# Optimization experiments

Hardware: AMD Instinct MI355X
Metric: run time of the kernel (lower is better)

The kernel has to match this reference:

```python
import jax, jax.numpy as jnp
import numpy as np

N, T, V, F, K, FO = 8, 64, 200, 64, 3, 64


def setup_inputs() -> dict:
    key = jax.random.key(0)
    k1, k2, k3, k4 = jax.random.split(key, 4)
    x = jax.random.normal(k1, (N, T, V, F), dtype=jnp.float32)
    Att = jax.random.uniform(k2, (N, V, V), dtype=jnp.float32)
    S = jax.random.uniform(k3, (N, T, V, V), dtype=jnp.float32)
    Theta = jax.random.normal(k4, (K, F, FO), dtype=jnp.float32) * 0.1
    return {"x": x, "Att": Att, "S": S, "Theta": Theta}


def reference(x, Att, S, Theta):
    # x: (N,T,V,F); Att: (N,V,V); S: (N,T,V,V); Theta: (K,F,FO)
    n, t, v, f = x.shape
    k_order = Theta.shape[0]
    # symmetrize S by elementwise min with its transpose (last two dims)
    S = jnp.minimum(S, jnp.swapaxes(S, -1, -2))
    eye = jnp.eye(v, dtype=x.dtype)
    # D = diag_embed(sum(A, dim=1)) per timestep -> column sums over axis 2
    d = jnp.sum(S, axis=2)                      # (N,T,V)
    L = d[..., :, None] * eye - S               # (N,T,V,V), D - A
    L_t = L - eye                               # tilde-L
    # Chebyshev recursion (elementwise, matching original code exactly)
    polys = [jnp.broadcast_to(eye, (1, 1, v, v)), L_t][:k_order]
    for _ in range(2, k_order):
        polys.append(2.0 * L_t * polys[-1] - polys[-2])
    Att_b = Att[:, None]                        # (N,1,V,V), broadcast over T
    out = jnp.zeros((n, t, v, Theta.shape[-1]), dtype=x.dtype)
    for kk in range(k_order):
        T_k_att = polys[kk] * Att_b             # (N,T,V,V) (broadcast for k=0)
        # rhs = T_k_att^T @ x : sum over vertex u
        rhs = jnp.einsum('...uv,...uf->...vf', T_k_att, x)  # (N,T,V,F)
        out = out + rhs @ Theta[kk]             # (N,T,V,FO)
    return jax.nn.relu(out)
```

## Files before the change

kernel.cpp:

```cpp
#include <hip/hip_runtime.h>

namespace {

typedef __attribute__((ext_vector_type(8)))  short          short8;
typedef __attribute__((ext_vector_type(8)))  unsigned short u16x8;
typedef __attribute__((ext_vector_type(4)))  unsigned short u16x4;
typedef __attribute__((ext_vector_type(4)))  float          f32x4;

constexpr int V   = 200;
constexpr int VP  = 208;
constexpr int UP  = 224;
constexpr int F   = 64;
constexpr int FO  = 64;
constexpr int NT  = 512;

constexpr int A_ROW = 448;

constexpr size_t WS_AC  = 0;
constexpr size_t WS_D   = 95420416;
constexpr size_t WS_SD  = 95846400;
constexpr size_t WS_AD  = 96272384;
constexpr size_t WS_THT = 96279552;

__device__ __forceinline__ unsigned short f2bf(float x) {
    union { float f; unsigned u; } c; c.f = x;
    unsigned r = c.u + 0x7FFF + ((c.u >> 16) & 1);
    return (unsigned short)(r >> 16);
}
__device__ __forceinline__ float bf2f(unsigned short h) {
    union { unsigned u; float f; } c; c.u = ((unsigned)h) << 16;
    return c.f;
}

__global__ __launch_bounds__(256)
void prep_A(const float* __restrict__ S,
            const float* __restrict__ Att,
            unsigned short* __restrict__ Ac,
            float* __restrict__ d_ws,
            float* __restrict__ sdiag)
{
    __shared__ float As[32][33];
    __shared__ float Bs[32][33];
    __shared__ float Ts[32][33];
    __shared__ float Us[32][33];

    const int b   = blockIdx.x;
    const int n   = b >> 6;
    const int tid = threadIdx.x;
    int rem = blockIdx.y, ti = 0;
    while (rem >= 7 - ti) { rem -= 7 - ti; ++ti; }
    const int tj = ti + rem;
    const bool diag = (ti == tj);

    const float* __restrict__ Sp = S   + (size_t)b * (V * V);
    const float* __restrict__ Ap = Att + (size_t)n * (V * V);

    const int r  = tid >> 3;
    const int cg = tid & 7;
    const int c0 = 4 * cg;

    {
        const int gr = 32 * ti + r, gc = 32 * tj + c0;
        float4 a = make_float4(0.f, 0.f, 0.f, 0.f);
        float4 t = make_float4(0.f, 0.f, 0.f, 0.f);
        if (gr < V && gc < V) {
            a = *(const float4*)&Sp[gr * V + gc];
            t = *(const float4*)&Ap[gr * V + gc];
        }
        As[r][c0 + 0] = a.x; As[r][c0 + 1] = a.y; As[r][c0 + 2] = a.z; As[r][c0 + 3] = a.w;
        Ts[r][c0 + 0] = t.x; Ts[r][c0 + 1] = t.y; Ts[r][c0 + 2] = t.z; Ts[r][c0 + 3] = t.w;
        if (!diag) {
            const int hr = 32 * tj + r, hc = 32 * ti + c0;
            float4 bb = make_float4(0.f, 0.f, 0.f, 0.f);
            float4 uu = make_float4(0.f, 0.f, 0.f, 0.f);
            if (hr < V && hc < V) {
                bb = *(const float4*)&Sp[hr * V + hc];
                uu = *(const float4*)&Ap[hr * V + hc];
            }
            Bs[r][c0 + 0] = bb.x; Bs[r][c0 + 1] = bb.y; Bs[r][c0 + 2] = bb.z; Bs[r][c0 + 3] = bb.w;
            Us[r][c0 + 0] = uu.x; Us[r][c0 + 1] = uu.y; Us[r][c0 + 2] = uu.z; Us[r][c0 + 3] = uu.w;
        }
    }
    __syncthreads();

    {
        const int vr = 32 * ti + r;
        float rs = 0.f;
        u16x4 w1, w2;
        #pragma unroll
        for (int e = 0; e < 4; ++e) {
            const int c = c0 + e;
            const float tw = diag ? As[c][r] : Bs[c][r];
            const float m  = fminf(As[r][c], tw);
            rs += m;
            const float att = diag ? Ts[c][r] : Us[c][r];
            float a1 = -m * att;
            float a2 = 2.0f * m * m * att;
            if (diag && r == c) { a1 = 0.f; a2 = 0.f; }
            w1[e] = f2bf(a1); w2[e] = f2bf(a2);
        }
        float s = rs;
        s += __shfl_xor(s, 1); s += __shfl_xor(s, 2); s += __shfl_xor(s, 4);
        if (cg == 0 && vr < V)
            atomicAdd(&d_ws[b * VP + vr], s);
        if (diag && cg == 0 && vr < V)
            sdiag[b * VP + vr] = As[r][r];
        if (vr < VP) {
            const size_t base = ((size_t)(b * VP + vr) * 7 + tj) * 64;
            *(u16x4*)&Ac[base + c0]      = w1;
            *(u16x4*)&Ac[base + 32 + c0] = w2;
        }
    }

    if (!diag) {
        const int vr2 = 32 * tj + r;
        float ts = 0.f;
        u16x4 w1, w2;
        #pragma unroll
        for (int e = 0; e < 4; ++e) {
            const int c = c0 + e;
            const float m = fminf(Bs[r][c], As[c][r]);
            ts += m;
            const float att = Ts[c][r];
            w1[e] = f2bf(-m * att);
            w2[e] = f2bf(2.0f * m * m * att);
        }
        float s = ts;
        s += __shfl_xor(s, 1); s += __shfl_xor(s, 2); s += __shfl_xor(s, 4);
        if (cg == 0 && vr2 < V)
            atomicAdd(&d_ws[b * VP + vr2], s);
        if (vr2 < VP) {
            const size_t base = ((size_t)(b * VP + vr2) * 7 + ti) * 64;
            *(u16x4*)&Ac[base + c0]      = w1;
            *(u16x4*)&Ac[base + 32 + c0] = w2;
        }
    }
}

__global__ __launch_bounds__(256)
void prep_adiag(const float* __restrict__ Att, float* __restrict__ adiag)
{
    const int n = blockIdx.x, tid = threadIdx.x;
    if (tid < UP)
        adiag[n * UP + tid] = (tid < V) ? Att[(size_t)n * (V * V) + tid * V + tid] : 0.f;
}

__global__ __launch_bounds__(256)
void prep_theta(const float* __restrict__ Theta,
                unsigned short* __restrict__ thT)
{
    __shared__ float T[64][65];
    const int k = blockIdx.x, tid = threadIdx.x;
    for (int idx = tid; idx < 4096; idx += 256)
        T[idx >> 6][idx & 63] = Theta[k * 4096 + idx];
    __syncthreads();
    for (int idx = tid; idx < 4096; idx += 256) {
        const int fo = idx >> 6, f = idx & 63;
        thT[k * 4096 + fo * 64 + f] = f2bf(T[f][fo]);
    }
}

constexpr int XS_S = 68;
constexpr int XT_S = 232;
constexpr int YS_S = 72;

__global__ __launch_bounds__(256, 2)
void cheb_main(const float* __restrict__ x,
               const unsigned short* __restrict__ thT,
               const unsigned short* __restrict__ Ac,
               const float* __restrict__ d_ws,
               const float* __restrict__ sdiag,
               const float* __restrict__ adiag,
               float* __restrict__ out)
{
    __shared__ __align__(16) char smem[61824];
    unsigned short* xsT = (unsigned short*)smem;
    unsigned short* xs  = (unsigned short*)(smem + 29696);
    unsigned short* ThS = (unsigned short*)smem;
    unsigned short* ys  = (unsigned short*)(smem + 29696);
    float*        cbuf  = (float*)(smem + 60160);
    float*       adbuf  = (float*)(smem + 60992);

    const int tid = threadIdx.x;
    const int b   = blockIdx.x;
    const int n   = b >> 6;
    const float* __restrict__ xp = x + (size_t)b * (V * F);
    const unsigned short* __restrict__ ap = Ac + (size_t)b * (VP * A_ROW);
    float* __restrict__ op = out + (size_t)b * (V * FO);

    for (int idx = tid; idx < UP * 16; idx += 256) {
        const int u = idx >> 4, fg = idx & 15;
        u16x4 w; w[0] = 0; w[1] = 0; w[2] = 0; w[3] = 0;
        if (u < V) {
            const float4 v = *(const float4*)&xp[u * F + 4 * fg];
            w[0] = f2bf(v.x); w[1] = f2bf(v.y); w[2] = f2bf(v.z); w[3] = f2bf(v.w);
        }
        *(u16x4*)&xs[u * XS_S + 4 * fg] = w;
    }
    if (tid < VP) {
        cbuf[tid]  = d_ws[b * VP + tid] - 1.0f - sdiag[b * VP + tid];
        adbuf[tid] = adiag[n * UP + tid];
    }
    __syncthreads();

    for (int it = 0; it < 7; ++it) {
        const int wid = tid + 256 * it;
        const int f = wid & 63, uc = wid >> 6;
        u16x8 w;
        #pragma unroll
        for (int j = 0; j < 8; ++j) w[j] = xs[(8 * uc + j) * XS_S + f];
        *(u16x8*)&xsT[f * XT_S + 8 * uc] = w;
    }
    __syncthreads();

    const int wave = tid >> 6, lane = tid & 63;
    const int q = lane >> 4, ln = lane & 15;
    const int myBase = (wave == 0) ? 0 : (4 + 3 * (wave - 1));
    const int myCnt  = (wave == 0) ? 4 : 3;

    f32x4 acc1[4][4], acc2[4][4];
    #pragma unroll
    for (int i = 0; i < 4; ++i)
        #pragma unroll
        for (int j = 0; j < 4; ++j) {
            acc1[i][j] = (f32x4)0.f; acc2[i][j] = (f32x4)0.f;
        }

    size_t rbase[4];
    #pragma unroll
    for (int vi = 0; vi < 4; ++vi)
        rbase[vi] = (size_t)((myBase + vi) * 16 + ln) * A_ROW;

    short8 a1c[4] = {}, a2c[4] = {}, a1n[4] = {}, a2n[4] = {};
    #pragma unroll
    for (int vi = 0; vi < 4; ++vi) if (vi < myCnt) {
        a1c[vi] = *(const short8*)&ap[rbase[vi] + 8 * q];
        a2c[vi] = *(const short8*)&ap[rbase[vi] + 32 + 8 * q];
    }
    #pragma unroll 1
    for (int kt = 0; kt < 7; ++kt) {
        if (kt < 6) {
            #pragma unroll
            for (int vi = 0; vi < 4; ++vi) if (vi < myCnt) {
                a1n[vi] = *(const short8*)&ap[rbase[vi] + (kt + 1) * 64 + 8 * q];
                a2n[vi] = *(const short8*)&ap[rbase[vi] + (kt + 1) * 64 + 32 + 8 * q];
            }
        }
        short8 bfr[4];
        #pragma unroll
        for (int ft = 0; ft < 4; ++ft)
            bfr[ft] = *(const short8*)&xsT[(16 * ft + ln) * XT_S + 32 * kt + 8 * q];
        #pragma unroll
        for (int vi = 0; vi < 4; ++vi) if (vi < myCnt) {
            #pragma unroll
            for (int ft = 0; ft < 4; ++ft) {
                acc1[vi][ft] = __builtin_amdgcn_mfma_f32_16x16x32_bf16(a1c[vi], bfr[ft], acc1[vi][ft], 0, 0, 0);
                acc2[vi][ft] = __builtin_amdgcn_mfma_f32_16x16x32_bf16(a2c[vi], bfr[ft], acc2[vi][ft], 0, 0, 0);
            }
        }
        #pragma unroll
        for (int vi = 0; vi < 4; ++vi) { a1c[vi] = a1n[vi]; a2c[vi] = a2n[vi]; }
    }

    f32x4 ot[4][4];
    #pragma unroll
    for (int i = 0; i < 4; ++i)
        #pragma unroll
        for (int j = 0; j < 4; ++j) ot[i][j] = (f32x4)0.f;

    #pragma unroll
    for (int pass = 0; pass < 3; ++pass) {
        const int k = (pass == 0) ? 1 : (pass == 1) ? 2 : 0;
        __syncthreads();

        if (k == 0) {
            for (int idx = tid; idx < VP * 16; idx += 256) {
                const int v = idx >> 4, fg = idx & 15;
                u16x4 w; w[0] = 0; w[1] = 0; w[2] = 0; w[3] = 0;
                if (v < V) {
                    const float av = adbuf[v];
                    const float4 xv = *(const float4*)&xp[v * F + 4 * fg];
                    w[0] = f2bf(av * xv.x); w[1] = f2bf(av * xv.y);
                    w[2] = f2bf(av * xv.z); w[3] = f2bf(av * xv.w);
                }
                *(u16x4*)&ys[v * YS_S + 4 * fg] = w;
            }
        } else {
            #pragma unroll
            for (int vi = 0; vi < 4; ++vi) {
                if (vi < myCnt) {
                    const int vt = myBase + vi;
                    #pragma unroll
                    for (int ft = 0; ft < 4; ++ft) {
                        const f32x4 a = (k == 1) ? acc1[vi][ft] : acc2[vi][ft];
                        #pragma unroll
                        for (int reg = 0; reg < 4; ++reg) {
                            const int v = vt * 16 + 4 * q + reg;
                            float val = 0.f;
                            if (v < V) {
                                const float cc = cbuf[v];
                                const float dc = ((k == 1) ? cc : (2.0f * cc * cc - 1.0f)) * adbuf[v];
                                val = a[reg] + dc * xp[v * F + 16 * ft + ln];
                            }
                            ys[v * YS_S + 16 * ft + ln] = f2bf(val);
                        }
                    }
                }
            }
        }
        for (int idx = tid; idx < 64 * 8; idx += 256) {
            const int fo = idx >> 3, ch = idx & 7;
            *(u16x8*)&ThS[fo * YS_S + 8 * ch] =
                *(const u16x8*)&thT[k * 4096 + fo * 64 + 8 * ch];
        }
        __syncthreads();
        #pragma unroll
        for (int vi = 0; vi < 4; ++vi) {
            if (vi < myCnt) {
                const int vrow = (myBase + vi) * 16 + ln;
                #pragma unroll
                for (int ks = 0; ks < 2; ++ks) {
                    const short8 af = *(const short8*)&ys[vrow * YS_S + 32 * ks + 8 * q];
                    #pragma unroll
                    for (int fot = 0; fot < 4; ++fot) {
                        const short8 bf = *(const short8*)&ThS[(16 * fot + ln) * YS_S + 32 * ks + 8 * q];
                        ot[vi][fot] = __builtin_amdgcn_mfma_f32_16x16x32_bf16(af, bf, ot[vi][fot], 0, 0, 0);
                    }
                }
            }
        }
    }

    #pragma unroll
    for (int vi = 0; vi < 4; ++vi) {
        if (vi < myCnt) {
            const int vt = myBase + vi;
            #pragma unroll
            for (int fot = 0; fot < 4; ++fot) {
                #pragma unroll
                for (int reg = 0; reg < 4; ++reg) {
                    const int v = vt * 16 + 4 * q + reg;
                    if (v < V)
                        op[v * FO + 16 * fot + ln] = fmaxf(ot[vi][fot][reg], 0.f);
                }
            }
        }
    }
}

}

extern "C" void kernel_launch(void* const* d_in, const int* in_sizes, int n_in,
                              void* d_out, int out_size, void* d_ws, size_t ws_size,
                              hipStream_t stream) {
    const float* x     = (const float*)d_in[0];
    const float* Att   = (const float*)d_in[1];
    const float* S     = (const float*)d_in[2];
    const float* Theta = (const float*)d_in[3];
    float* out         = (float*)d_out;

    char* ws = (char*)d_ws;
    unsigned short* Ac  = (unsigned short*)(ws + WS_AC);
    float* d_sum        = (float*)(ws + WS_D);
    float* sdiag        = (float*)(ws + WS_SD);
    float* adiag        = (float*)(ws + WS_AD);
    unsigned short* thT = (unsigned short*)(ws + WS_THT);

    hipMemsetAsync(d_sum, 0, (size_t)NT * VP * sizeof(float), stream);

    hipLaunchKernelGGL(prep_A,     dim3(NT, 28), dim3(256), 0, stream, S, Att, Ac, d_sum, sdiag);
    hipLaunchKernelGGL(prep_adiag, dim3(8),      dim3(256), 0, stream, Att, adiag);
    hipLaunchKernelGGL(prep_theta, dim3(3),      dim3(256), 0, stream, Theta, thT);
    hipLaunchKernelGGL(cheb_main,  dim3(NT),     dim3(256), 0, stream,
                       x, thT, Ac, d_sum, sdiag, adiag, out);
}
```

Measured before the change: 247.5 us.

## Fuse Laplacian/attention prep into main Chebyshev kernel, split vertices across two blocks

The separate prep_A pass, which wrote a large bf16 A matrix to workspace along with atomically summed degrees, is removed. Each block of the fused kernel now reads S and Att tiles directly, symmetrises them, builds the bf16 A1/A2 tiles in LDS and accumulates degree sums per 32-column chunk before issuing MFMAs. Each timestep is split across two blocks by vertex half, with smaller LDS and accumulator sets, targeting occupancy 4. x transposition and Theta preparation are merged into one small prep kernel. This avoids the workspace round-trip and the memset, but each block re-reads its S columns, and Att is read with strided scalar loads.

```diff
diff --git a/kernel.cpp b/kernel.cpp
--- a/kernel.cpp
+++ b/kernel.cpp
@@ -7,264 +7,205 @@
 typedef __attribute__((ext_vector_type(4)))  unsigned short u16x4;
 typedef __attribute__((ext_vector_type(4)))  float          f32x4;
 
-constexpr int V   = 200;
-constexpr int VP  = 208;
-constexpr int UP  = 224;
-constexpr int F   = 64;
-constexpr int FO  = 64;
-constexpr int NT  = 512;
-
-constexpr int A_ROW = 448;
-
-constexpr size_t WS_AC  = 0;
-constexpr size_t WS_D   = 95420416;
-constexpr size_t WS_SD  = 95846400;
-constexpr size_t WS_AD  = 96272384;
-constexpr size_t WS_THT = 96279552;
+constexpr int V  = 200;
+constexpr int F  = 64;
+constexpr int NT = 512;
+
+constexpr size_t WS_XT  = 0;
+constexpr size_t WS_THT = 14680064;
 
 __device__ __forceinline__ unsigned short f2bf(float x) {
     union { float f; unsigned u; } c; c.f = x;
     unsigned r = c.u + 0x7FFF + ((c.u >> 16) & 1);
     return (unsigned short)(r >> 16);
 }
-__device__ __forceinline__ float bf2f(unsigned short h) {
-    union { unsigned u; float f; } c; c.u = ((unsigned)h) << 16;
-    return c.f;
-}
 
 __global__ __launch_bounds__(256)
-void prep_A(const float* __restrict__ S,
-            const float* __restrict__ Att,
-            unsigned short* __restrict__ Ac,
-            float* __restrict__ d_ws,
-            float* __restrict__ sdiag)
+void prep_misc(const float* __restrict__ x,
+               const float* __restrict__ Theta,
+               unsigned short* __restrict__ xT,
+               unsigned short* __restrict__ thT)
 {
-    __shared__ float As[32][33];
-    __shared__ float Bs[32][33];
-    __shared__ float Ts[32][33];
-    __shared__ float Us[32][33];
-
-    const int b   = blockIdx.x;
-    const int n   = b >> 6;
+    __shared__ __align__(16) char smem[30464];
+    const int bb = blockIdx.x, tid = threadIdx.x;
+    if (bb < NT) {
+        unsigned short* xs = (unsigned short*)smem;
+        const float* __restrict__ xp = x + (size_t)bb * (V * F);
+        for (int idx = tid; idx < 224 * 16; idx += 256) {
+            const int u = idx >> 4, fg = idx & 15;
+            u16x4 w; w[0] = 0; w[1] = 0; w[2] = 0; w[3] = 0;
+            if (u < V) {
+                const float4 v4 = *(const float4*)&xp[u * F + 4 * fg];
+                w[0] = f2bf(v4.x); w[1] = f2bf(v4.y); w[2] = f2bf(v4.z); w[3] = f2bf(v4.w);
+            }
+            *(u16x4*)&xs[u * 68 + 4 * fg] = w;
+        }
+        __syncthreads();
+        unsigned short* xo = xT + (size_t)bb * (64 * 224);
+        for (int it = 0; it < 8; ++it) {
+            const int wid = tid + 256 * it;
+            const int f = wid >> 5, sl = wid & 31;
+            if (sl < 28) {
+                u16x8 w;
+                #pragma unroll
+                for (int j = 0; j < 8; ++j) w[j] = xs[(8 * sl + j) * 68 + f];
+                *(u16x8*)&xo[f * 224 + 8 * sl] = w;
+            }
+        }
+    } else {
+        float* T = (float*)smem;
+        for (int k = 0; k < 3; ++k) {
+            __syncthreads();
+            for (int idx = tid; idx < 4096; idx += 256)
+                T[(idx >> 6) * 65 + (idx & 63)] = Theta[k * 4096 + idx];
+            __syncthreads();
+            for (int idx = tid; idx < 4096; idx += 256) {
+                const int fo = idx >> 6, f = idx & 63;
+                thT[k * 4096 + fo * 64 + f] = f2bf(T[f * 65 + fo]);
+            }
+        }
+    }
+}
+
+__global__ __launch_bounds__(256, 4)
+void cheb_fused(const float* __restrict__ x,
+                const float* __restrict__ S,
+                const float* __restrict__ Att,
+                const unsigned short* __restrict__ thT,
+                const unsigned short* __restrict__ xT,
+                float* __restrict__ out)
+{
+    __shared__ __align__(16) char smem[30208];
+    float*          sru = (float*)smem;
+    unsigned short* A1  = (unsigned short*)(smem + 14464);
+    unsigned short* A2  = (unsigned short*)(smem + 21632);
+    unsigned short* ys  = (unsigned short*)smem;
+    unsigned short* ThS = (unsigned short*)(smem + 16128);
+    float* dbuf = (float*)(smem + 28800);
+    float* sdb  = (float*)(smem + 29248);
+    float* adb  = (float*)(smem + 29696);
+
     const int tid = threadIdx.x;
-    int rem = blockIdx.y, ti = 0;
-    while (rem >= 7 - ti) { rem -= 7 - ti; ++ti; }
-    const int tj = ti + rem;
-    const bool diag = (ti == tj);
-
-    const float* __restrict__ Sp = S   + (size_t)b * (V * V);
-    const float* __restrict__ Ap = Att + (size_t)n * (V * V);
-
-    const int r  = tid >> 3;
-    const int cg = tid & 7;
-    const int c0 = 4 * cg;
-
-    {
-        const int gr = 32 * ti + r, gc = 32 * tj + c0;
-        float4 a = make_float4(0.f, 0.f, 0.f, 0.f);
-        float4 t = make_float4(0.f, 0.f, 0.f, 0.f);
-        if (gr < V && gc < V) {
-            a = *(const float4*)&Sp[gr * V + gc];
-            t = *(const float4*)&Ap[gr * V + gc];
-        }
-        As[r][c0 + 0] = a.x; As[r][c0 + 1] = a.y; As[r][c0 + 2] = a.z; As[r][c0 + 3] = a.w;
-        Ts[r][c0 + 0] = t.x; Ts[r][c0 + 1] = t.y; Ts[r][c0 + 2] = t.z; Ts[r][c0 + 3] = t.w;
-        if (!diag) {
-            const int hr = 32 * tj + r, hc = 32 * ti + c0;
-            float4 bb = make_float4(0.f, 0.f, 0.f, 0.f);
-            float4 uu = make_float4(0.f, 0.f, 0.f, 0.f);
-            if (hr < V && hc < V) {
-                bb = *(const float4*)&Sp[hr * V + hc];
-                uu = *(const float4*)&Ap[hr * V + hc];
-            }
-            Bs[r][c0 + 0] = bb.x; Bs[r][c0 + 1] = bb.y; Bs[r][c0 + 2] = bb.z; Bs[r][c0 + 3] = bb.w;
-            Us[r][c0 + 0] = uu.x; Us[r][c0 + 1] = uu.y; Us[r][c0 + 2] = uu.z; Us[r][c0 + 3] = uu.w;
-        }
-    }
+    const int b = blockIdx.x >> 1, h = blockIdx.x & 1;
+    const int n = b >> 6;
+    const int v0 = h * 112;
+    const int NVL = h ? 96 : 112;
+    const int NV4 = NVL >> 2;
+
+    const float* __restrict__ Sp  = S   + (size_t)b * (V * V);
+    const float* __restrict__ Ap  = Att + (size_t)n * (V * V);
+    const float* __restrict__ xp  = x   + (size_t)b * (V * F);
+    const unsigned short* __restrict__ xTp = xT + (size_t)b * (64 * 224);
+    float* __restrict__ op = out + (size_t)b * (V * F);
+
+    if (tid < 112) { dbuf[tid] = 0.f; sdb[tid] = 0.f; adb[tid] = 0.f; }
+
+    const int wave = tid >> 6, lane = tid & 63, q = lane >> 4, ln = lane & 15;
+    int myBase, myCnt;
+    if (h == 0) { myCnt = (wave < 3) ? 2 : 1; myBase = 2 * wave; }
+    else        { myCnt = (wave < 2) ? 2 : 1; myBase = (wave < 2) ? 2 * wave : 2 + wave; }
+
+    f32x4 acc1[2][4], acc2[2][4];
+    #pragma unroll
+    for (int i = 0; i < 2; ++i)
+        #pragma unroll
+        for (int j = 0; j < 4; ++j) { acc1[i][j] = (f32x4)0.f; acc2[i][j] = (f32x4)0.f; }
+
+    float4 spf[4];
+    auto load_sru = [&](int kt) {
+        #pragma unroll
+        for (int c = 0; c < 4; ++c) {
+            const int idx = tid + 256 * c;
+            const int ul = idx >> 5, sl = idx & 31;
+            const int u = 32 * kt + ul, vv = v0 + 4 * sl;
+            float4 z = make_float4(0.f, 0.f, 0.f, 0.f);
+            if (sl < NV4 && u < V && vv < V)
+                z = *(const float4*)&Sp[u * V + vv];
+            spf[c] = z;
+        }
+    };
+    load_sru(0);
     __syncthreads();
 
-    {
-        const int vr = 32 * ti + r;
-        float rs = 0.f;
-        u16x4 w1, w2;
-        #pragma unroll
-        for (int e = 0; e < 4; ++e) {
-            const int c = c0 + e;
-            const float tw = diag ? As[c][r] : Bs[c][r];
-            const float m  = fminf(As[r][c], tw);
-            rs += m;
-            const float att = diag ? Ts[c][r] : Us[c][r];
-            float a1 = -m * att;
-            float a2 = 2.0f * m * m * att;
-            if (diag && r == c) { a1 = 0.f; a2 = 0.f; }
-            w1[e] = f2bf(a1); w2[e] = f2bf(a2);
-        }
-        float s = rs;
-        s += __shfl_xor(s, 1); s += __shfl_xor(s, 2); s += __shfl_xor(s, 4);
-        if (cg == 0 && vr < V)
-            atomicAdd(&d_ws[b * VP + vr], s);
-        if (diag && cg == 0 && vr < V)
-            sdiag[b * VP + vr] = As[r][r];
-        if (vr < VP) {
-            const size_t base = ((size_t)(b * VP + vr) * 7 + tj) * 64;
-            *(u16x4*)&Ac[base + c0]      = w1;
-            *(u16x4*)&Ac[base + 32 + c0] = w2;
-        }
-    }
-
-    if (!diag) {
-        const int vr2 = 32 * tj + r;
-        float ts = 0.f;
-        u16x4 w1, w2;
-        #pragma unroll
-        for (int e = 0; e < 4; ++e) {
-            const int c = c0 + e;
-            const float m = fminf(Bs[r][c], As[c][r]);
-            ts += m;
-            const float att = Ts[c][r];
-            w1[e] = f2bf(-m * att);
-            w2[e] = f2bf(2.0f * m * m * att);
-        }
-        float s = ts;
-        s += __shfl_xor(s, 1); s += __shfl_xor(s, 2); s += __shfl_xor(s, 4);
-        if (cg == 0 && vr2 < V)
-            atomicAdd(&d_ws[b * VP + vr2], s);
-        if (vr2 < VP) {
-            const size_t base = ((size_t)(b * VP + vr2) * 7 + ti) * 64;
-            *(u16x4*)&Ac[base + c0]      = w1;
-            *(u16x4*)&Ac[base + 32 + c0] = w2;
-        }
-    }
-}
-
-__global__ __launch_bounds__(256)
-void prep_adiag(const float* __restrict__ Att, float* __restrict__ adiag)
-{
-    const int n = blockIdx.x, tid = threadIdx.x;
-    if (tid < UP)
-        adiag[n * UP + tid] = (tid < V) ? Att[(size_t)n * (V * V) + tid * V + tid] : 0.f;
-}
-
-__global__ __launch_bounds__(256)
-void prep_theta(const float* __restrict__ Theta,
-                unsigned short* __restrict__ thT)
-{
-    __shared__ float T[64][65];
-    const int k = blockIdx.x, tid = threadIdx.x;
-    for (int idx = tid; idx < 4096; idx += 256)
-        T[idx >> 6][idx & 63] = Theta[k * 4096 + idx];
-    __syncthreads();
-    for (int idx = tid; idx < 4096; idx += 256) {
-        const int fo = idx >> 6, f = idx & 63;
-        thT[k * 4096 + fo * 64 + f] = f2bf(T[f][fo]);
-    }
-}
-
-constexpr int XS_S = 68;
-constexpr int XT_S = 232;
-constexpr int YS_S = 72;
-
-__global__ __launch_bounds__(256, 2)
-void cheb_main(const float* __restrict__ x,
-               const unsigned short* __restrict__ thT,
-               const unsigned short* __restrict__ Ac,
-               const float* __restrict__ d_ws,
-               const float* __restrict__ sdiag,
-               const float* __restrict__ adiag,
-               float* __restrict__ out)
-{
-    __shared__ __align__(16) char smem[61824];
-    unsigned short* xsT = (unsigned short*)smem;
-    unsigned short* xs  = (unsigned short*)(smem + 29696);
-    unsigned short* ThS = (unsigned short*)smem;
-    unsigned short* ys  = (unsigned short*)(smem + 29696);
-    float*        cbuf  = (float*)(smem + 60160);
-    float*       adbuf  = (float*)(smem + 60992);
-
-    const int tid = threadIdx.x;
-    const int b   = blockIdx.x;
-    const int n   = b >> 6;
-    const float* __restrict__ xp = x + (size_t)b * (V * F);
-    const unsigned short* __restrict__ ap = Ac + (size_t)b * (VP * A_ROW);
-    float* __restrict__ op = out + (size_t)b * (V * FO);
-
-    for (int idx = tid; idx < UP * 16; idx += 256) {
-        const int u = idx >> 4, fg = idx & 15;
-        u16x4 w; w[0] = 0; w[1] = 0; w[2] = 0; w[3] = 0;
-        if (u < V) {
-            const float4 v = *(const float4*)&xp[u * F + 4 * fg];
-            w[0] = f2bf(v.x); w[1] = f2bf(v.y); w[2] = f2bf(v.z); w[3] = f2bf(v.w);
-        }
-        *(u16x4*)&xs[u * XS_S + 4 * fg] = w;
-    }
-    if (tid < VP) {
-        cbuf[tid]  = d_ws[b * VP + tid] - 1.0f - sdiag[b * VP + tid];
-        adbuf[tid] = adiag[n * UP + tid];
-    }
-    __syncthreads();
-
-    for (int it = 0; it < 7; ++it) {
-        const int wid = tid + 256 * it;
-        const int f = wid & 63, uc = wid >> 6;
-        u16x8 w;
-        #pragma unroll
-        for (int j = 0; j < 8; ++j) w[j] = xs[(8 * uc + j) * XS_S + f];
-        *(u16x8*)&xsT[f * XT_S + 8 * uc] = w;
-    }
-    __syncthreads();
-
-    const int wave = tid >> 6, lane = tid & 63;
-    const int q = lane >> 4, ln = lane & 15;
-    const int myBase = (wave == 0) ? 0 : (4 + 3 * (wave - 1));
-    const int myCnt  = (wave == 0) ? 4 : 3;
-
-    f32x4 acc1[4][4], acc2[4][4];
-    #pragma unroll
-    for (int i = 0; i < 4; ++i)
-        #pragma unroll
-        for (int j = 0; j < 4; ++j) {
-            acc1[i][j] = (f32x4)0.f; acc2[i][j] = (f32x4)0.f;
-        }
-
-    size_t rbase[4];
-    #pragma unroll
-    for (int vi = 0; vi < 4; ++vi)
-        rbase[vi] = (size_t)((myBase + vi) * 16 + ln) * A_ROW;
-
-    short8 a1c[4] = {}, a2c[4] = {}, a1n[4] = {}, a2n[4] = {};
-    #pragma unroll
-    for (int vi = 0; vi < 4; ++vi) if (vi < myCnt) {
-        a1c[vi] = *(const short8*)&ap[rbase[vi] + 8 * q];
-        a2c[vi] = *(const short8*)&ap[rbase[vi] + 32 + 8 * q];
-    }
     #pragma unroll 1
     for (int kt = 0; kt < 7; ++kt) {
-        if (kt < 6) {
-            #pragma unroll
-            for (int vi = 0; vi < 4; ++vi) if (vi < myCnt) {
-                a1n[vi] = *(const short8*)&ap[rbase[vi] + (kt + 1) * 64 + 8 * q];
-                a2n[vi] = *(const short8*)&ap[rbase[vi] + (kt + 1) * 64 + 32 + 8 * q];
-            }
-        }
-        short8 bfr[4];
+        #pragma unroll
+        for (int c = 0; c < 4; ++c) {
+            const int idx = tid + 256 * c;
+            const int ul = idx >> 5, sl = idx & 31;
+            if (sl < NV4) *(float4*)&sru[ul * 113 + 4 * sl] = spf[c];
+        }
+        __syncthreads();
+
+        short8 bcur[4];
         #pragma unroll
         for (int ft = 0; ft < 4; ++ft)
-            bfr[ft] = *(const short8*)&xsT[(16 * ft + ln) * XT_S + 32 * kt + 8 * q];
-        #pragma unroll
-        for (int vi = 0; vi < 4; ++vi) if (vi < myCnt) {
-            #pragma unroll
-            for (int ft = 0; ft < 4; ++ft) {
-                acc1[vi][ft] = __builtin_amdgcn_mfma_f32_16x16x32_bf16(a1c[vi], bfr[ft], acc1[vi][ft], 0, 0, 0);
-                acc2[vi][ft] = __builtin_amdgcn_mfma_f32_16x16x32_bf16(a2c[vi], bfr[ft], acc2[vi][ft], 0, 0, 0);
-            }
-        }
-        #pragma unroll
-        for (int vi = 0; vi < 4; ++vi) { a1c[vi] = a1n[vi]; a2c[vi] = a2n[vi]; }
+            bcur[ft] = *(const short8*)&xTp[(16 * ft + ln) * 224 + 32 * kt + 8 * q];
+        #pragma unroll
+        for (int c = 0; c < 4; ++c) {
+            const int idx = tid + 256 * c;
+            if (idx < NVL * 8) {
+                const int vl = idx >> 3, ug = idx & 7;
+                const int v = v0 + vl;
+                const bool vok = v < V;
+                const int u0 = 32 * kt + 4 * ug;
+                float4 sc = make_float4(0.f, 0.f, 0.f, 0.f);
+                if (vok && u0 < V) sc = *(const float4*)&Sp[v * V + u0];
+                float rs = 0.f;
+                u16x4 w1, w2;
+                #pragma unroll
+                for (int j = 0; j < 4; ++j) {
+                    const int u = u0 + j;
+                    const bool ok = vok && (u < V);
+                    float att = 0.f, srt = 0.f;
+                    if (ok) {
+                        att = Ap[u * V + v];
+                        srt = sru[(4 * ug + j) * 113 + vl];
+                    }
+                    const float scj = (j == 0) ? sc.x : (j == 1) ? sc.y : (j == 2) ? sc.z : sc.w;
+                    float m = fminf(scj, srt);
+                    if (!ok) m = 0.f;
+                    rs += m;
+                    float a1, a2;
+                    if (u == v) {
+                        a1 = 0.f; a2 = 0.f;
+                        if (vok) { sdb[vl] = m; adb[vl] = att; }
+                    } else {
+                        a1 = -m * att;
+                        a2 = 2.0f * m * m * att;
+                    }
+                    w1[j] = f2bf(a1); w2[j] = f2bf(a2);
+                }
+                *(u16x4*)&A1[vl * 32 + 4 * ug] = w1;
+                *(u16x4*)&A2[vl * 32 + 4 * ug] = w2;
+                rs += __shfl_xor(rs, 1); rs += __shfl_xor(rs, 2); rs += __shfl_xor(rs, 4);
+                if (ug == 0 && vok) dbuf[vl] += rs;
+            }
+        }
+        if (kt < 6) load_sru(kt + 1);
+        __syncthreads();
+
+        #pragma unroll
+        for (int vi = 0; vi < 2; ++vi) {
+            if (vi < myCnt) {
+                const int row = (myBase + vi) * 16 + ln;
+                const short8 af1 = *(const short8*)&A1[row * 32 + 8 * q];
+                const short8 af2 = *(const short8*)&A2[row * 32 + 8 * q];
+                #pragma unroll
+                for (int ft = 0; ft < 4; ++ft) {
+                    acc1[vi][ft] = __builtin_amdgcn_mfma_f32_16x16x32_bf16(af1, bcur[ft], acc1[vi][ft], 0, 0, 0);
+                    acc2[vi][ft] = __builtin_amdgcn_mfma_f32_16x16x32_bf16(af2, bcur[ft], acc2[vi][ft], 0, 0, 0);
+                }
+            }
+        }
     }
 
-    f32x4 ot[4][4];
+    __syncthreads();
+    if (tid < 112) dbuf[tid] = dbuf[tid] - 1.0f - sdb[tid];
+
+    f32x4 ot[2][4];
     #pragma unroll
-    for (int i = 0; i < 4; ++i)
+    for (int i = 0; i < 2; ++i)
         #pragma unroll
         for (int j = 0; j < 4; ++j) ot[i][j] = (f32x4)0.f;
 
@@ -274,56 +215,58 @@
         __syncthreads();
 
         if (k == 0) {
-            for (int idx = tid; idx < VP * 16; idx += 256) {
-                const int v = idx >> 4, fg = idx & 15;
+            for (int idx = tid; idx < NVL * 16; idx += 256) {
+                const int vl = idx >> 4, fg = idx & 15;
+                const int v = v0 + vl;
                 u16x4 w; w[0] = 0; w[1] = 0; w[2] = 0; w[3] = 0;
                 if (v < V) {
-                    const float av = adbuf[v];
+                    const float av = adb[vl];
                     const float4 xv = *(const float4*)&xp[v * F + 4 * fg];
                     w[0] = f2bf(av * xv.x); w[1] = f2bf(av * xv.y);
                     w[2] = f2bf(av * xv.z); w[3] = f2bf(av * xv.w);
                 }
-                *(u16x4*)&ys[v * YS_S + 4 * fg] = w;
+                *(u16x4*)&ys[vl * 72 + 4 * fg] = w;
             }
         } else {
             #pragma unroll
-            for (int vi = 0; vi < 4; ++vi) {
+            for (int vi = 0; vi < 2; ++vi) {
                 if (vi < myCnt) {
-                    const int vt = myBase + vi;
+                    const int lt = myBase + vi;
                     #pragma unroll
                     for (int ft = 0; ft < 4; ++ft) {
                         const f32x4 a = (k == 1) ? acc1[vi][ft] : acc2[vi][ft];
                         #pragma unroll
                         for (int reg = 0; reg < 4; ++reg) {
-                            const int v = vt * 16 + 4 * q + reg;
+                            const int vl = lt * 16 + 4 * q + reg;
+                            const int v = v0 + vl;
                             float val = 0.f;
                             if (v < V) {
-                                const float cc = cbuf[v];
-                                const float dc = ((k == 1) ? cc : (2.0f * cc * cc - 1.0f)) * adbuf[v];
+                                const float cc = dbuf[vl];
+                                const float dc = ((k == 1) ? cc : (2.0f * cc * cc - 1.0f)) * adb[vl];
                                 val = a[reg] + dc * xp[v * F + 16 * ft + ln];
                             }
-                            ys[v * YS_S + 16 * ft + ln] = f2bf(val);
+                            ys[vl * 72 + 16 * ft + ln] = f2bf(val);
                         }
                     }
                 }
             }
         }
-        for (int idx = tid; idx < 64 * 8; idx += 256) {
+        for (int idx = tid; idx < 512; idx += 256) {
             const int fo = idx >> 3, ch = idx & 7;
-            *(u16x8*)&ThS[fo * YS_S + 8 * ch] =
+            *(u16x8*)&ThS[fo * 72 + 8 * ch] =
                 *(const u16x8*)&thT[k * 4096 + fo * 64 + 8 * ch];
         }
         __syncthreads();
         #pragma unroll
-        for (int vi = 0; vi < 4; ++vi) {
+        for (int vi = 0; vi < 2; ++vi) {
             if (vi < myCnt) {
                 const int vrow = (myBase + vi) * 16 + ln;
                 #pragma unroll
                 for (int ks = 0; ks < 2; ++ks) {
-                    const short8 af = *(const short8*)&ys[vrow * YS_S + 32 * ks + 8 * q];
+                    const short8 af = *(const short8*)&ys[vrow * 72 + 32 * ks + 8 * q];
                     #pragma unroll
                     for (int fot = 0; fot < 4; ++fot) {
-                        const short8 bf = *(const short8*)&ThS[(16 * fot + ln) * YS_S + 32 * ks + 8 * q];
+                        const short8 bf = *(const short8*)&ThS[(16 * fot + ln) * 72 + 32 * ks + 8 * q];
                         ot[vi][fot] = __builtin_amdgcn_mfma_f32_16x16x32_bf16(af, bf, ot[vi][fot], 0, 0, 0);
                     }
                 }
@@ -332,16 +275,16 @@
     }
 
     #pragma unroll
-    for (int vi = 0; vi < 4; ++vi) {
+    for (int vi = 0; vi < 2; ++vi) {
         if (vi < myCnt) {
-            const int vt = myBase + vi;
+            const int lt = myBase + vi;
             #pragma unroll
             for (int fot = 0; fot < 4; ++fot) {
                 #pragma unroll
                 for (int reg = 0; reg < 4; ++reg) {
-                    const int v = vt * 16 + 4 * q + reg;
+                    const int v = v0 + lt * 16 + 4 * q + reg;
                     if (v < V)
-                        op[v * FO + 16 * fot + ln] = fmaxf(ot[vi][fot][reg], 0.f);
+                        op[v * F + 16 * fot + ln] = fmaxf(ot[vi][fot][reg], 0.f);
                 }
             }
         }
@@ -360,17 +303,10 @@
     float* out         = (float*)d_out;
 
     char* ws = (char*)d_ws;
-    unsigned short* Ac  = (unsigned short*)(ws + WS_AC);
-    float* d_sum        = (float*)(ws + WS_D);
-    float* sdiag        = (float*)(ws + WS_SD);
-    float* adiag        = (float*)(ws + WS_AD);
+    unsigned short* xT  = (unsigned short*)(ws + WS_XT);
     unsigned short* thT = (unsigned short*)(ws + WS_THT);
 
-    hipMemsetAsync(d_sum, 0, (size_t)NT * VP * sizeof(float), stream);
-
-    hipLaunchKernelGGL(prep_A,     dim3(NT, 28), dim3(256), 0, stream, S, Att, Ac, d_sum, sdiag);
-    hipLaunchKernelGGL(prep_adiag, dim3(8),      dim3(256), 0, stream, Att, adiag);
-    hipLaunchKernelGGL(prep_theta, dim3(3),      dim3(256), 0, stream, Theta, thT);
-    hipLaunchKernelGGL(cheb_main,  dim3(NT),     dim3(256), 0, stream,
-                       x, thT, Ac, d_sum, sdiag, adiag, out);
-}
+    hipLaunchKernelGGL(prep_misc,  dim3(NT + 1), dim3(256), 0, stream, x, Theta, xT, thT);
+    hipLaunchKernelGGL(cheb_fused, dim3(2 * NT), dim3(256), 0, stream,
+                       x, S, Att, thT, xT, out);
+}
```

Result: slower. 344.8 us (+39.3%).
